# Optimization experiments

Measured on AMD Instinct MI355X. Metric: run time of the kernel, lower is better.

Reference implementation:

```python
import jax, jax.numpy as jnp
import numpy as np

NEG_INF = -jnp.inf


def setup_inputs() -> dict:
    B, V = 128, 128000
    key = jax.random.key(0)
    k1, k2, k3, k4, k5 = jax.random.split(key, 5)
    logits = jax.random.normal(k1, (B, V), dtype=jnp.float32)
    # temperatures in [0.1, 1.0) to avoid divide-by-tiny blowups
    temperatures = jax.random.uniform(k2, (B,), dtype=jnp.float32) * 0.9 + 0.1
    # min_p typically small, in [0, 0.1)
    min_ps = jax.random.uniform(k3, (B,), dtype=jnp.float32) * 0.1
    # top_p in [0.1, 1.0)
    top_ps = jax.random.uniform(k4, (B,), dtype=jnp.float32) * 0.9 + 0.1
    # top_k in [1, 1000)
    top_ks = jax.random.randint(k5, (B,), 1, 1000, dtype=jnp.int32)
    return {"logits": logits, "temperatures": temperatures, "min_ps": min_ps,
            "top_ps": top_ps, "top_ks": top_ks}


def _apply_top_k_top_p(logits, top_ps, top_ks):
    B, V = logits.shape
    sort_idx = jnp.argsort(logits, axis=-1)  # ascending, matches torch sort(descending=False)
    logits_sort = jnp.take_along_axis(logits, sort_idx, axis=-1)
    # top-k: threshold is the (V-k)-th smallest value; mask anything strictly below it
    thresh_idx = (V - top_ks.astype(jnp.int32))[:, None]          # [B,1]
    thresh = jnp.take_along_axis(logits_sort, thresh_idx, axis=-1)  # [B,1]
    logits_sort = jnp.where(logits_sort < thresh, NEG_INF, logits_sort)
    # top-p: drop smallest tokens whose cumulative prob <= 1 - p; never drop the max token
    probs_sort = jax.nn.softmax(logits_sort, axis=-1)
    probs_sum = jnp.cumsum(probs_sort, axis=-1)
    top_p_mask = probs_sum <= (1.0 - top_ps)[:, None]
    top_p_mask = top_p_mask.at[:, -1].set(False)
    logits_sort = jnp.where(top_p_mask, NEG_INF, logits_sort)
    # scatter back to original vocab order
    rows = jnp.arange(B)[:, None]
    return jnp.zeros_like(logits_sort).at[rows, sort_idx].set(logits_sort)


def _apply_min_p(logits, min_ps):
    probs = jax.nn.softmax(logits, axis=-1)
    top_probs = jnp.max(probs, axis=-1, keepdims=True)
    remove = probs < min_ps[:, None] * top_probs
    return jnp.where(remove, NEG_INF, logits)


def reference(logits, temperatures, min_ps, top_ps, top_ks):
    logits = logits.astype(jnp.float32) / temperatures[:, None]
    logits = _apply_top_k_top_p(logits, top_ps, top_ks)
    logits = _apply_min_p(logits, min_ps)
    # torch.multinomial(softmax(logits), 1) == categorical sampling from logits
    sample_key = jax.random.key(42)
    next_tokens = jax.random.categorical(sample_key, logits, axis=-1)  # [B]
    return next_tokens
```

## Files before the change

### kernel.cpp

```cpp
#include <hip/hip_runtime.h>
#include <stdint.h>

#define HBINS 8192
#define HSHIFT 19
#define CAND 2048
#define NSLICES 16
#define HTHREADS 256
#define CTHREADS 256
#define STHREADS 1024

typedef unsigned int u32;
typedef unsigned long long u64;

__device__ __forceinline__ u32 f2s(float f) {
  u32 b = __float_as_uint(f);
  return b ^ ((b & 0x80000000u) ? 0xFFFFFFFFu : 0x80000000u);
}
__device__ __forceinline__ float s2f(u32 s) {
  u32 b = (s & 0x80000000u) ? (s ^ 0x80000000u) : ~s;
  return __uint_as_float(b);
}
__device__ __forceinline__ u32 rotl32(u32 x, int r) { return (x << r) | (x >> (32 - r)); }

__device__ __forceinline__ u64 shfl_xor_u64(u64 v, int mask) {
  int lo = __shfl_xor((int)(u32)v, mask, 64);
  int hi = __shfl_xor((int)(u32)(v >> 32), mask, 64);
  return ((u64)(u32)hi << 32) | (u32)lo;
}

__device__ __forceinline__ u32 threefry_bits(u32 ctr) {
  const u32 ks0 = 0u, ks1 = 42u, ks2 = 0x1BD11BDAu ^ 0u ^ 42u;
  u32 x0 = ks0;
  u32 x1 = ctr + ks1;
#define TFR(r) { x0 += x1; x1 = rotl32(x1, (r)); x1 ^= x0; }
  TFR(13) TFR(15) TFR(26) TFR(6)   x0 += ks1; x1 += ks2 + 1u;
  TFR(17) TFR(29) TFR(16) TFR(24)  x0 += ks2; x1 += ks0 + 2u;
  TFR(13) TFR(15) TFR(26) TFR(6)   x0 += ks0; x1 += ks1 + 3u;
  TFR(17) TFR(29) TFR(16) TFR(24)  x0 += ks1; x1 += ks2 + 4u;
  TFR(13) TFR(15) TFR(26) TFR(6)   x0 += ks2; x1 += ks0 + 5u;
#undef TFR
  return x0 ^ x1;
}

__global__ __launch_bounds__(1024)
void zero_kernel(u32* __restrict__ p, int n) {
  int i = blockIdx.x * 1024 + threadIdx.x;
  if (i < n) p[i] = 0u;
}

__global__ __launch_bounds__(HTHREADS)
void hist_kernel(const float* __restrict__ logits, u32* __restrict__ ghist,
                 int V, int slice_len) {
  const int row = blockIdx.x / NSLICES;
  const int sl  = blockIdx.x % NSLICES;
  const int tid = threadIdx.x;
  __shared__ u32 hp[HBINS];
  for (int i = tid; i < HBINS; i += HTHREADS) hp[i] = 0u;
  __syncthreads();
  int rem = V - sl * slice_len;
  if (rem > slice_len) rem = slice_len;
  if (rem < 0) rem = 0;
  const float* src = logits + (size_t)row * (size_t)V + (size_t)sl * slice_len;
  const u32 c = (u32)(tid & 1);
  const int n4 = rem >> 2;
  const float4* p4 = (const float4*)src;
  for (int i = tid; i < n4; i += HTHREADS) {
    float4 w = p4[i];
    u32 b0 = f2s(w.x) >> HSHIFT;
    u32 b1 = f2s(w.y) >> HSHIFT;
    u32 b2 = f2s(w.z) >> HSHIFT;
    u32 b3 = f2s(w.w) >> HSHIFT;
    atomicAdd(&hp[(b0 & ~1u) | c], 1u << ((b0 & 1u) << 4));
    atomicAdd(&hp[(b1 & ~1u) | c], 1u << ((b1 & 1u) << 4));
    atomicAdd(&hp[(b2 & ~1u) | c], 1u << ((b2 & 1u) << 4));
    atomicAdd(&hp[(b3 & ~1u) | c], 1u << ((b3 & 1u) << 4));
  }
  for (int i = (n4 << 2) + tid; i < rem; i += HTHREADS) {
    u32 b = f2s(src[i]) >> HSHIFT;
    atomicAdd(&hp[(b & ~1u) | c], 1u << ((b & 1u) << 4));
  }
  __syncthreads();
  u32* gh = ghist + (size_t)row * HBINS;
  for (int p = tid; p < HBINS / 2; p += HTHREADS) {
    u32 s = hp[2 * p] + hp[2 * p + 1];
    if (s) {
      u32 lo = s & 0xFFFFu;
      u32 hi = s >> 16;
      if (lo) atomicAdd(&gh[2 * p], lo);
      if (hi) atomicAdd(&gh[2 * p + 1], hi);
    }
  }
}

__global__ __launch_bounds__(256)
void select_kernel(const u32* __restrict__ ghist, const int* __restrict__ topks,
                   u32* __restrict__ gthr, u32* __restrict__ gcs,
                   u32* __restrict__ gcount, int V) {
  const int row = blockIdx.x;
  const int tid = threadIdx.x;
  __shared__ u32 hist[HBINS];
  __shared__ u32 part[256];
  __shared__ u32 chunk[64];
  const u32* gh = ghist + (size_t)row * HBINS;
  for (int i = tid; i < HBINS; i += 256) hist[i] = gh[i];
  __syncthreads();
  {
    u32 s = 0;
    for (int j = 0; j < 32; ++j) s += hist[tid * 32 + j];
    part[tid] = s;
  }
  __syncthreads();
  if (tid < 64) {
    chunk[tid] = part[tid * 4] + part[tid * 4 + 1] + part[tid * 4 + 2] + part[tid * 4 + 3];
  }
  __syncthreads();
  if (tid == 0) {
    int k = topks[row];
    if (k < 1) k = 1;
    if (k > V) k = V;
    const u32 ku = (u32)k;
    u32 acc = 0;
    int cstar = 0;
    for (int c = 63; c >= 0; --c) {
      if (acc + chunk[c] >= ku) { cstar = c; break; }
      acc += chunk[c];
    }
    int pstar = cstar * 4;
    for (int p = cstar * 4 + 3; p >= cstar * 4; --p) {
      if (acc + part[p] >= ku) { pstar = p; break; }
      acc += part[p];
    }
    int bstar = pstar * 32;
    for (int bq = pstar * 32 + 31; bq >= pstar * 32; --bq) {
      acc += hist[bq];
      if (acc >= ku) { bstar = bq; break; }
    }
    gthr[row] = (u32)bstar << HSHIFT;
    gcs[row] = (acc < (u32)CAND ? acc : (u32)CAND);
    gcount[row] = 0u;
  }
}

__global__ __launch_bounds__(CTHREADS)
void collect_kernel(const float* __restrict__ logits,
                    const float* __restrict__ temps,
                    const u32* __restrict__ gthr,
                    u32* __restrict__ gcount,
                    u64* __restrict__ gcand, int V, int slice_len) {
  const int row = blockIdx.x / NSLICES;
  const int sl  = blockIdx.x % NSLICES;
  const int tid = threadIdx.x;

  __shared__ u64 stage[CAND];
  __shared__ int sh_cnt, sh_base;
  if (tid == 0) sh_cnt = 0;
  __syncthreads();

  const u32 thr = gthr[row];
  const float t = temps[row];
  int rem = V - sl * slice_len;
  if (rem > slice_len) rem = slice_len;
  if (rem < 0) rem = 0;
  const float* src = logits + (size_t)row * (size_t)V + (size_t)sl * slice_len;
  const u32 ibase = (u32)(sl * slice_len);
  const int n4 = rem >> 2;
  const float4* p4 = (const float4*)src;
  for (int i = tid; i < n4; i += CTHREADS) {
    float4 w = p4[i];
    if (f2s(w.x) >= thr) { int pos = atomicAdd(&sh_cnt, 1); if (pos < CAND) stage[pos] = ((u64)f2s(w.x / t) << 32) | (ibase + 4u * i + 0u); }
    if (f2s(w.y) >= thr) { int pos = atomicAdd(&sh_cnt, 1); if (pos < CAND) stage[pos] = ((u64)f2s(w.y / t) << 32) | (ibase + 4u * i + 1u); }
    if (f2s(w.z) >= thr) { int pos = atomicAdd(&sh_cnt, 1); if (pos < CAND) stage[pos] = ((u64)f2s(w.z / t) << 32) | (ibase + 4u * i + 2u); }
    if (f2s(w.w) >= thr) { int pos = atomicAdd(&sh_cnt, 1); if (pos < CAND) stage[pos] = ((u64)f2s(w.w / t) << 32) | (ibase + 4u * i + 3u); }
  }
  for (int i = (n4 << 2) + tid; i < rem; i += CTHREADS) {
    float l = src[i];
    if (f2s(l) >= thr) { int pos = atomicAdd(&sh_cnt, 1); if (pos < CAND) stage[pos] = ((u64)f2s(l / t) << 32) | (ibase + (u32)i); }
  }
  __syncthreads();
  int n = sh_cnt;
  if (n > CAND) n = CAND;
  if (tid == 0) sh_base = (int)atomicAdd(&gcount[row], (u32)n);
  __syncthreads();
  const int base = sh_base;
  u64* gc = gcand + (size_t)row * CAND;
  for (int i = tid; i < n; i += CTHREADS) {
    int dst = base + i;
    if (dst < CAND) gc[dst] = stage[i];
  }
}

__global__ __launch_bounds__(STHREADS)
void Sampler_73529840107542_kernel(const float* __restrict__ minps,
                                   const float* __restrict__ topps,
                                   const int* __restrict__ topks,
                                   const u32* __restrict__ gcs,
                                   const u64* __restrict__ gcand,
                                   int* __restrict__ out, int V) {
  const int b = blockIdx.x;
  const int tid = threadIdx.x;
  const int w = tid >> 6;
  const int l = tid & 63;
  const float one_minus_p = 1.0f - topps[b];
  const float minp = minps[b];
  int k = topks[b];
  if (k < 1) k = 1;
  if (k > V) k = V;

  __shared__ __align__(16) unsigned char arena[34816];
  u64* cand   = (u64*)(arena);
  float* bufA = (float*)(arena + 16384);
  float* bufB = (float*)(arena + 24576);
  unsigned char* keepf = arena + 32768;
  u64* red64  = (u64*)(arena + 16384);
  float* redA = (float*)(arena + 16384);
  float* redB = (float*)(arena + 24576);

  __shared__ int sh_lb;
  __shared__ u32 sh_Ts;
  __shared__ float sh_m, sh_Z1, sh_Z2;

  const int cs = (int)gcs[b];
  const u64* gc = gcand + (size_t)b * CAND;
  const int e_lo = (w << 7) + l;
  const int e_hi = e_lo + 64;
  const u64 SENT = 0xFFFFFFFFFFFFFFFFull;
  u64 k0 = (e_lo < cs) ? gc[e_lo] : SENT;
  u64 k1 = (e_hi < cs) ? gc[e_hi] : SENT;

  int P = 64;
  while (P < cs) P <<= 1;
  for (int size = 2; size <= P; size <<= 1) {
    for (int s = size >> 1; s > 0; s >>= 1) {
      if (s >= 128) {
        cand[e_lo] = k0; cand[e_hi] = k1;
        __syncthreads();
        u64 p0 = cand[e_lo ^ s], p1 = cand[e_hi ^ s];
        {
          bool keepmin = (((e_lo & s) == 0) == ((e_lo & size) == 0));
          if (keepmin ? (p0 < k0) : (p0 > k0)) k0 = p0;
        }
        {
          bool keepmin = (((e_hi & s) == 0) == ((e_hi & size) == 0));
          if (keepmin ? (p1 < k1) : (p1 > k1)) k1 = p1;
        }
        __syncthreads();
      } else if (s == 64) {
        bool asc = ((e_lo & size) == 0);
        if ((k0 > k1) == asc) { u64 t = k0; k0 = k1; k1 = t; }
      } else {
        u64 p0 = shfl_xor_u64(k0, s);
        u64 p1 = shfl_xor_u64(k1, s);
        {
          bool keepmin = (((l & s) == 0) == ((e_lo & size) == 0));
          if (keepmin ? (p0 < k0) : (p0 > k0)) k0 = p0;
        }
        {
          bool keepmin = (((l & s) == 0) == ((e_hi & size) == 0));
          if (keepmin ? (p1 < k1) : (p1 > k1)) k1 = p1;
        }
      }
    }
  }
  cand[e_lo] = k0; cand[e_hi] = k1;
  __syncthreads();

  if (tid == 0) {
    int ti = cs - k; if (ti < 0) ti = 0;
    sh_Ts = (u32)(cand[ti] >> 32);
    sh_m  = s2f((u32)(cand[cs - 1] >> 32));
  }
  __syncthreads();
  const u32 Ts = sh_Ts;
  const float m = sh_m;

  for (int c = tid; c < cs; c += STHREADS) {
    u32 s = (u32)(cand[c] >> 32);
    if (s >= Ts && (c == 0 || (u32)(cand[c - 1] >> 32) < Ts)) sh_lb = c;
  }
  __syncthreads();
  const int lb = sh_lb;

  for (int c = tid; c < CAND; c += STHREADS) {
    float e = 0.0f;
    if (c < cs) {
      u32 s = (u32)(cand[c] >> 32);
      if (s >= Ts) e = expf(s2f(s) - m);
    }
    bufA[c] = e;
  }
  __syncthreads();

  {
    float local = bufA[tid] + bufA[tid + STHREADS];
    redB[tid] = local;
    __syncthreads();
    for (int s = STHREADS >> 1; s > 0; s >>= 1) {
      if (tid < s) redB[tid] += redB[tid + s];
      __syncthreads();
    }
    if (tid == 0) sh_Z1 = redB[0];
    __syncthreads();
  }

  const float Z1 = sh_Z1;
  for (int c = tid; c < CAND; c += STHREADS) bufA[c] = bufA[c] / Z1;
  __syncthreads();

  if (w == 0) {
    float carry = 0.0f;
    for (int base = lb; base < cs; base += 64) {
      int c = base + l;
      float v = (c < cs) ? bufA[c] : 0.0f;
      u32 vb = __float_as_uint(v);
      float acc = carry;
#pragma unroll
      for (int j = 0; j < 64; ++j) {
        float t = __uint_as_float(__builtin_amdgcn_readlane(vb, j));
        acc += (l >= j) ? t : 0.0f;
      }
      if (c < cs) bufB[c] = acc;
      carry = __uint_as_float(__builtin_amdgcn_readlane(__float_as_uint(acc), 63));
    }
  }
  __syncthreads();

  for (int c = tid; c < CAND; c += STHREADS) {
    unsigned char kf = 0;
    if (c < cs) {
      u32 s = (u32)(cand[c] >> 32);
      if (s >= Ts && (c == cs - 1 || bufB[c] > one_minus_p)) kf = 1;
    }
    keepf[c] = kf;
  }
  __syncthreads();

  {
    float local = 0.0f;
    for (int c = tid; c < CAND; c += STHREADS) {
      if (keepf[c]) {
        u32 s = (u32)(cand[c] >> 32);
        local += expf(s2f(s) - m);
      }
    }
    redA[tid] = local;
    __syncthreads();
    for (int s = STHREADS >> 1; s > 0; s >>= 1) {
      if (tid < s) redA[tid] += redA[tid + s];
      __syncthreads();
    }
    if (tid == 0) sh_Z2 = redA[0];
    __syncthreads();
  }

  {
    const float Z2 = sh_Z2;
    const float rhs = minp * (1.0f / Z2);
    for (int c = tid; c < CAND; c += STHREADS) {
      if (keepf[c]) {
        u32 s = (u32)(cand[c] >> 32);
        float p2 = expf(s2f(s) - m) / Z2;
        if (p2 < rhs) keepf[c] = 0;
      }
    }
  }
  __syncthreads();

  {
    const float TINY = 1.17549435082228750797e-38f;
    u64 best = 0ull;
    for (int c = lb + tid; c < cs; c += STHREADS) {
      if (!keepf[c]) continue;
      u32 s = (u32)(cand[c] >> 32);
      u32 idx = (u32)(cand[c] & 0xFFFFFFFFull);
      float x = s2f(s);
      u32 bits = threefry_bits((u32)b * (u32)V + idx);
      float f = __uint_as_float((bits >> 9) | 0x3f800000u) - 1.0f;
      float u = fmaxf(TINY, f * 1.0f + TINY);
      float g = -logf(-logf(u));
      float sc = g + x;
      u64 key = ((u64)f2s(sc) << 32) | (u64)(0xFFFFFFFFu - idx);
      if (key > best) best = key;
    }
    red64[tid] = best;
    __syncthreads();
    for (int s = STHREADS >> 1; s > 0; s >>= 1) {
      if (tid < s) { u64 o = red64[tid + s]; if (o > red64[tid]) red64[tid] = o; }
      __syncthreads();
    }
    if (tid == 0) out[b] = (int)(0xFFFFFFFFu - (u32)(red64[0] & 0xFFFFFFFFull));
  }
}

extern "C" void kernel_launch(void* const* d_in, const int* in_sizes, int n_in,
                              void* d_out, int out_size, void* d_ws, size_t ws_size,
                              hipStream_t stream) {
  const float* logits = (const float*)d_in[0];
  const float* temps  = (const float*)d_in[1];
  const float* minps  = (const float*)d_in[2];
  const float* topps  = (const float*)d_in[3];
  const int*   topks  = (const int*)d_in[4];
  const int B = in_sizes[1];
  const int V = in_sizes[0] / B;
  (void)n_in; (void)out_size; (void)ws_size;

  u32* ghist  = (u32*)d_ws;
  u32* gcount = ghist + (size_t)B * HBINS;
  u32* gcs    = gcount + B;
  u32* gthr   = gcs + B;
  u64* gcand  = (u64*)(gthr + B);

  const int nz = B * HBINS;
  const int slice_len = (((V + NSLICES - 1) / NSLICES) + 3) & ~3;

  zero_kernel<<<dim3((nz + 1023) / 1024), dim3(1024), 0, stream>>>(ghist, nz);
  hist_kernel<<<dim3(B * NSLICES), dim3(HTHREADS), 0, stream>>>(logits, ghist, V, slice_len);
  select_kernel<<<dim3(B), dim3(256), 0, stream>>>(ghist, topks, gthr, gcs, gcount, V);
  collect_kernel<<<dim3(B * NSLICES), dim3(CTHREADS), 0, stream>>>(
      logits, temps, gthr, gcount, gcand, V, slice_len);
  Sampler_73529840107542_kernel<<<dim3(B), dim3(STHREADS), 0, stream>>>(
      minps, topps, topks, gcs, gcand, (int*)d_out, V);
}
```

Measured before the change: 170.2 us.

## Fuse histogram and threshold selection via last-block-done pattern

Merges the histogram and select kernels into one launch: each slice block adds its partial histogram to global memory, and the last block to finish a row (tracked by an atomic done counter) does the top-k bin search with a parallel suffix scan. The zero kernel is replaced by hipMemsetAsync, and the shared histogram drops the two-copy interleave, halving shared memory. This removes two launches and a serial scan in exchange for extra fences and atomics, and more shared-atomic contention now that all threads share one copy.

```diff
diff --git a/kernel.cpp b/kernel.cpp
--- a/kernel.cpp
+++ b/kernel.cpp
@@ -3,6 +3,7 @@
 
 #define HBINS 8192
 #define HSHIFT 19
+#define HWORDS (HBINS / 2)
 #define CAND 2048
 #define NSLICES 16
 #define HTHREADS 256
@@ -42,26 +43,25 @@
   return x0 ^ x1;
 }
 
-__global__ __launch_bounds__(1024)
-void zero_kernel(u32* __restrict__ p, int n) {
-  int i = blockIdx.x * 1024 + threadIdx.x;
-  if (i < n) p[i] = 0u;
-}
-
 __global__ __launch_bounds__(HTHREADS)
-void hist_kernel(const float* __restrict__ logits, u32* __restrict__ ghist,
-                 int V, int slice_len) {
+void histsel_kernel(const float* __restrict__ logits, u32* __restrict__ ghist,
+                    u32* __restrict__ done, const int* __restrict__ topks,
+                    u32* __restrict__ gthr, u32* __restrict__ gcs,
+                    u32* __restrict__ gcount, int V, int slice_len) {
   const int row = blockIdx.x / NSLICES;
   const int sl  = blockIdx.x % NSLICES;
   const int tid = threadIdx.x;
-  __shared__ u32 hp[HBINS];
-  for (int i = tid; i < HBINS; i += HTHREADS) hp[i] = 0u;
-  __syncthreads();
+  __shared__ u32 hp[HWORDS];
+  __shared__ u32 part[HTHREADS];
+  __shared__ int sh_last, sh_pstar;
+
+  for (int i = tid; i < HWORDS; i += HTHREADS) hp[i] = 0u;
+  __syncthreads();
+
   int rem = V - sl * slice_len;
   if (rem > slice_len) rem = slice_len;
   if (rem < 0) rem = 0;
   const float* src = logits + (size_t)row * (size_t)V + (size_t)sl * slice_len;
-  const u32 c = (u32)(tid & 1);
   const int n4 = rem >> 2;
   const float4* p4 = (const float4*)src;
   for (int i = tid; i < n4; i += HTHREADS) {
@@ -70,19 +70,20 @@
     u32 b1 = f2s(w.y) >> HSHIFT;
     u32 b2 = f2s(w.z) >> HSHIFT;
     u32 b3 = f2s(w.w) >> HSHIFT;
-    atomicAdd(&hp[(b0 & ~1u) | c], 1u << ((b0 & 1u) << 4));
-    atomicAdd(&hp[(b1 & ~1u) | c], 1u << ((b1 & 1u) << 4));
-    atomicAdd(&hp[(b2 & ~1u) | c], 1u << ((b2 & 1u) << 4));
-    atomicAdd(&hp[(b3 & ~1u) | c], 1u << ((b3 & 1u) << 4));
+    atomicAdd(&hp[b0 >> 1], 1u << ((b0 & 1u) << 4));
+    atomicAdd(&hp[b1 >> 1], 1u << ((b1 & 1u) << 4));
+    atomicAdd(&hp[b2 >> 1], 1u << ((b2 & 1u) << 4));
+    atomicAdd(&hp[b3 >> 1], 1u << ((b3 & 1u) << 4));
   }
   for (int i = (n4 << 2) + tid; i < rem; i += HTHREADS) {
     u32 b = f2s(src[i]) >> HSHIFT;
-    atomicAdd(&hp[(b & ~1u) | c], 1u << ((b & 1u) << 4));
-  }
-  __syncthreads();
+    atomicAdd(&hp[b >> 1], 1u << ((b & 1u) << 4));
+  }
+  __syncthreads();
+
   u32* gh = ghist + (size_t)row * HBINS;
-  for (int p = tid; p < HBINS / 2; p += HTHREADS) {
-    u32 s = hp[2 * p] + hp[2 * p + 1];
+  for (int p = tid; p < HWORDS; p += HTHREADS) {
+    u32 s = hp[p];
     if (s) {
       u32 lo = s & 0xFFFFu;
       u32 hi = s >> 16;
@@ -90,54 +91,63 @@
       if (hi) atomicAdd(&gh[2 * p + 1], hi);
     }
   }
-}
-
-__global__ __launch_bounds__(256)
-void select_kernel(const u32* __restrict__ ghist, const int* __restrict__ topks,
-                   u32* __restrict__ gthr, u32* __restrict__ gcs,
-                   u32* __restrict__ gcount, int V) {
-  const int row = blockIdx.x;
-  const int tid = threadIdx.x;
-  __shared__ u32 hist[HBINS];
-  __shared__ u32 part[256];
-  __shared__ u32 chunk[64];
-  const u32* gh = ghist + (size_t)row * HBINS;
-  for (int i = tid; i < HBINS; i += 256) hist[i] = gh[i];
-  __syncthreads();
-  {
-    u32 s = 0;
-    for (int j = 0; j < 32; ++j) s += hist[tid * 32 + j];
-    part[tid] = s;
-  }
-  __syncthreads();
-  if (tid < 64) {
-    chunk[tid] = part[tid * 4] + part[tid * 4 + 1] + part[tid * 4 + 2] + part[tid * 4 + 3];
-  }
-  __syncthreads();
+  __syncthreads();
+
   if (tid == 0) {
-    int k = topks[row];
-    if (k < 1) k = 1;
-    if (k > V) k = V;
-    const u32 ku = (u32)k;
-    u32 acc = 0;
-    int cstar = 0;
-    for (int c = 63; c >= 0; --c) {
-      if (acc + chunk[c] >= ku) { cstar = c; break; }
-      acc += chunk[c];
-    }
-    int pstar = cstar * 4;
-    for (int p = cstar * 4 + 3; p >= cstar * 4; --p) {
-      if (acc + part[p] >= ku) { pstar = p; break; }
-      acc += part[p];
-    }
-    int bstar = pstar * 32;
-    for (int bq = pstar * 32 + 31; bq >= pstar * 32; --bq) {
-      acc += hist[bq];
-      if (acc >= ku) { bstar = bq; break; }
-    }
-    gthr[row] = (u32)bstar << HSHIFT;
-    gcs[row] = (acc < (u32)CAND ? acc : (u32)CAND);
-    gcount[row] = 0u;
+    __threadfence();
+    u32 old = atomicAdd(&done[row], 1u);
+    sh_last = (old == (u32)(NSLICES - 1));
+  }
+  __syncthreads();
+  if (!sh_last) return;
+
+  __threadfence();
+  int k = topks[row];
+  if (k < 1) k = 1;
+  if (k > V) k = V;
+  const u32 ku = (u32)k;
+
+  u32 base = 0;
+  for (int h = 1; h >= 0; --h) {
+    __syncthreads();
+    for (int i = tid; i < 4096; i += HTHREADS)
+      hp[i] = __hip_atomic_load(&gh[h * 4096 + i], __ATOMIC_RELAXED,
+                                __HIP_MEMORY_SCOPE_AGENT);
+    __syncthreads();
+    {
+      u32 s = 0;
+      for (int j = 0; j < 16; ++j) s += hp[tid * 16 + j];
+      part[tid] = s;
+    }
+    __syncthreads();
+    for (int st = 1; st < HTHREADS; st <<= 1) {
+      u32 v = (tid + st < HTHREADS) ? part[tid + st] : 0u;
+      __syncthreads();
+      part[tid] += v;
+      __syncthreads();
+    }
+    const u32 tot = part[0];
+    if (base + tot >= ku) {
+      if (base + part[tid] >= ku &&
+          (tid == HTHREADS - 1 || base + part[tid + 1] < ku))
+        sh_pstar = tid;
+      __syncthreads();
+      const int pstar = sh_pstar;
+      const u32 tail = base + ((pstar < HTHREADS - 1) ? part[pstar + 1] : 0u);
+      if (tid < 16) {
+        u32 sb = tail;
+        for (int j = 15; j >= tid; --j) sb += hp[pstar * 16 + j];
+        u32 sb_next = sb - hp[pstar * 16 + tid];
+        if (sb >= ku && (tid == 15 || sb_next < ku)) {
+          int bstar = h * 4096 + pstar * 16 + tid;
+          gthr[row] = (u32)bstar << HSHIFT;
+          gcs[row] = (sb < (u32)CAND) ? sb : (u32)CAND;
+          gcount[row] = 0u;
+        }
+      }
+      return;
+    }
+    base += tot;
   }
 }
 
@@ -404,17 +414,17 @@
   (void)n_in; (void)out_size; (void)ws_size;
 
   u32* ghist  = (u32*)d_ws;
-  u32* gcount = ghist + (size_t)B * HBINS;
+  u32* done   = ghist + (size_t)B * HBINS;
+  u32* gcount = done + B;
   u32* gcs    = gcount + B;
   u32* gthr   = gcs + B;
   u64* gcand  = (u64*)(gthr + B);
 
-  const int nz = B * HBINS;
   const int slice_len = (((V + NSLICES - 1) / NSLICES) + 3) & ~3;
 
-  zero_kernel<<<dim3((nz + 1023) / 1024), dim3(1024), 0, stream>>>(ghist, nz);
-  hist_kernel<<<dim3(B * NSLICES), dim3(HTHREADS), 0, stream>>>(logits, ghist, V, slice_len);
-  select_kernel<<<dim3(B), dim3(256), 0, stream>>>(ghist, topks, gthr, gcs, gcount, V);
+  (void)hipMemsetAsync(ghist, 0, ((size_t)B * HBINS + B) * sizeof(u32), stream);
+  histsel_kernel<<<dim3(B * NSLICES), dim3(HTHREADS), 0, stream>>>(
+      logits, ghist, done, topks, gthr, gcs, gcount, V, slice_len);
   collect_kernel<<<dim3(B * NSLICES), dim3(CTHREADS), 0, stream>>>(
       logits, temps, gthr, gcount, gcand, V, slice_len);
   Sampler_73529840107542_kernel<<<dim3(B), dim3(STHREADS), 0, stream>>>(
```

Result: slower. 239.0 us (+40.4%).
